# Performance work log

Hardware: AMD Instinct MI355X
Metric: run time of the kernel (lower is better)

Reference implementation:

```python
import jax, jax.numpy as jnp
import numpy as np

# Model dims (mamba-2.8b-ish layer, single 8192-token prefill)
H, I, N, R, K, L = 2048, 4096, 16, 128, 4, 8192


def setup_inputs() -> dict:
    key = jax.random.key(0)
    ks = jax.random.split(key, 7)
    return {
        "hidden_states": jax.random.normal(ks[0], (L, H), jnp.float32),
        "W_in": jax.random.normal(ks[1], (H, 2 * I), jnp.float32) * 0.02,   # in_proj (no bias)
        "conv_w": jax.random.normal(ks[2], (I, K), jnp.float32) * 0.2,      # depthwise conv weight
        "conv_b": jnp.zeros((I,), jnp.float32),                              # use_conv_bias=True
        "W_x": jax.random.normal(ks[3], (I, R + 2 * N), jnp.float32) * 0.02, # x_proj (no bias)
        "W_dt": jax.random.normal(ks[4], (R, I), jnp.float32) * 0.01,        # dt_proj weight
        "dt_bias": jax.random.normal(ks[5], (I,), jnp.float32) * 0.1,        # dt_proj bias (delta_bias)
        "A_log": jnp.log(jnp.broadcast_to(jnp.arange(1, N + 1, dtype=jnp.float32), (I, N))) + 0.0,
        "D": jnp.ones((I,), jnp.float32),
        "W_out": jax.random.normal(ks[6], (I, H), jnp.float32) * 0.02,       # out_proj (no bias)
    }


def silu(x):
    return x * jax.nn.sigmoid(x)


def causal_dw_conv(x, w, b):
    # x: [L, I]; depthwise causal conv along time (padding K-1, left only)
    xt = x.T[None]  # [1, I, L] (NCW)
    y = jax.lax.conv_general_dilated(xt, w[:, None, :], (1,), [(K - 1, 0)],
                                     feature_group_count=I)  # [1, I, L]
    return y[0].T + b


def mamba_forward(hidden_states, W_in, conv_w, conv_b, W_x, W_dt, dt_bias, A_log, D, W_out):
    proj = hidden_states @ W_in                     # [L, 2I]
    x, gate = proj[:, :I], proj[:, I:]
    x = silu(causal_dw_conv(x, conv_w, conv_b))     # causal_conv1d_fn with silu
    ssm = x @ W_x                                   # [L, R+2N]
    dt_lr, B, C = ssm[:, :R], ssm[:, R:R + N], ssm[:, R + N:]
    delta = jax.nn.softplus(dt_lr @ W_dt + dt_bias) # delta_softplus=True with delta_bias
    A = -jnp.exp(A_log)                             # [I, N]

    def step(h, t):
        d_t, B_t, C_t, u_t = t                      # [I], [N], [N], [I]
        h = h * jnp.exp(d_t[:, None] * A) + (d_t * u_t)[:, None] * B_t[None, :]
        return h, h @ C_t                           # y_t: [I]

    h0 = jnp.zeros((I, N), jnp.float32)
    _, y = jax.lax.scan(step, h0, (delta, B, C, x)) # y: [L, I]
    y = (y + x * D) * silu(gate)                    # skip D*u and z-gating (selective_scan_fn)
    return y @ W_out                                # out_proj -> [L, H]


def reference(hidden_states, W_in, conv_w, conv_b, W_x, W_dt, dt_bias, A_log, D, W_out):
    return mamba_forward(hidden_states, W_in, conv_w, conv_b, W_x, W_dt, dt_bias, A_log, D, W_out)
```

## Files before the change

### kernel.cpp

```cpp
#include <hip/hip_runtime.h>
#include <cmath>
#include <stdint.h>

#define H_DIM 2048
#define I_DIM 4096
#define N_DIM 16
#define R_DIM 128
#define K_CONV 4
#define L_DIM 8192
#define LC 2048
#define NCHUNK (L_DIM / LC)
#define SEG 32
#define TSEG (LC / SEG)
#define IN_DIM (I_DIM * N_DIM)

typedef _Float16 f16x8 __attribute__((ext_vector_type(8)));
typedef _Float16 f16x4v __attribute__((ext_vector_type(4)));
typedef float    f32x4 __attribute__((ext_vector_type(4)));

__device__ __forceinline__ void gl_lds(const _Float16* g, _Float16* lbase, int lane) {
#if __has_builtin(__builtin_amdgcn_global_load_lds)
    __builtin_amdgcn_global_load_lds(
        (const __attribute__((address_space(1))) void*)g,
        (__attribute__((address_space(3))) void*)lbase, 16, 0, 0);
#else
    *(f16x8*)&lbase[lane * 8] = *(const f16x8*)g;
#endif
}

template <int OUTF16>
__global__ __launch_bounds__(512, 1) void gemm_p256(
    const _Float16* __restrict__ Aph,
    const _Float16* __restrict__ Bph,
    void* __restrict__ Cv, int ldc, int Kd, int gm,
    int kchunk, size_t partStride)
{
    __shared__ __align__(16) _Float16 Sh[3][2][8192];

    const int tid = threadIdx.x;
    int bid = blockIdx.x;
    const int q = gridDim.x >> 3;
    bid = (bid & 7) * q + (bid >> 3);
    const int m0 = (bid % gm) * 256;
    const int n0 = (bid / gm) * 256;

    const int kbeg = blockIdx.y * kchunk;

    const int w = tid >> 6, l = tid & 63;
    const int wm = w & 3, wn = w >> 2;
    const int lr = l & 15, lg = l >> 4;

    const int KP = Kd >> 5;
    const int np0 = n0 >> 4, mp0 = m0 >> 4;
    const int st0 = w;

    f32x4 acc[4][8];
#pragma unroll
    for (int a = 0; a < 4; ++a)
#pragma unroll
        for (int b = 0; b < 8; ++b) acc[a][b] = (f32x4){0.f, 0.f, 0.f, 0.f};

    auto stage = [&](int k0, int p) {
        const int kp = k0 >> 5;
#pragma unroll
        for (int s = 0; s < 2; ++s) {
            const int st = st0 + s * 8;
            gl_lds(Aph + ((size_t)(mp0 + st) * KP + kp) * 512 + (size_t)l * 8,
                   &Sh[p][0][st * 512], l);
            gl_lds(Bph + ((size_t)(np0 + st) * KP + kp) * 512 + (size_t)l * 8,
                   &Sh[p][1][st * 512], l);
        }
    };
    auto domfma = [&](int b) {
        f16x8 fah[4];
#pragma unroll
        for (int t = 0; t < 4; ++t)
            fah[t] = *(const f16x8*)&Sh[b][0][(wm * 4 + t) * 512 + l * 8];
        __builtin_amdgcn_s_setprio(1);
#pragma unroll
        for (int nh = 0; nh < 2; ++nh) {
            f16x8 fbh[4];
#pragma unroll
            for (int t = 0; t < 4; ++t)
                fbh[t] = *(const f16x8*)&Sh[b][1][(wn * 8 + nh * 4 + t) * 512 + l * 8];
#pragma unroll
            for (int mt = 0; mt < 4; ++mt)
#pragma unroll
                for (int nt = 0; nt < 4; ++nt)
                    acc[mt][nh * 4 + nt] = __builtin_amdgcn_mfma_f32_16x16x32_f16(
                        fah[mt], fbh[nt], acc[mt][nh * 4 + nt], 0, 0, 0);
        }
        __builtin_amdgcn_s_setprio(0);
    };

    const int KT = kchunk >> 5;
    stage(kbeg, 0);
    stage(kbeg + 32, 1);
    for (int k = 0; k + 2 < KT; ++k) {
        stage(kbeg + (k + 2) * 32, (k + 2) % 3);
        asm volatile("s_waitcnt vmcnt(8)" ::: "memory");
        __builtin_amdgcn_s_barrier();
        __builtin_amdgcn_sched_barrier(0);
        domfma(k % 3);
        __builtin_amdgcn_s_barrier();
    }
    asm volatile("s_waitcnt vmcnt(4)" ::: "memory");
    __builtin_amdgcn_s_barrier();
    __builtin_amdgcn_sched_barrier(0);
    domfma((KT - 2) % 3);
    __builtin_amdgcn_s_barrier();
    asm volatile("s_waitcnt vmcnt(0)" ::: "memory");
    __builtin_amdgcn_s_barrier();
    __builtin_amdgcn_sched_barrier(0);
    domfma((KT - 1) % 3);

#pragma unroll
    for (int mt = 0; mt < 4; ++mt) {
        const int row = m0 + wm * 64 + mt * 16 + lg * 4;
#pragma unroll
        for (int nt = 0; nt < 8; ++nt) {
            const int col = n0 + wn * 128 + nt * 16 + lr;
#pragma unroll
            for (int j = 0; j < 4; ++j) {
                if (OUTF16) {
                    _Float16* C = (_Float16*)Cv + (size_t)blockIdx.y * partStride;
                    C[(size_t)(row + j) * ldc + col] = (_Float16)acc[mt][nt][j];
                } else {
                    float* C = (float*)Cv + (size_t)blockIdx.y * partStride;
                    C[(size_t)(row + j) * ldc + col] = acc[mt][nt][j];
                }
            }
        }
    }
}

__global__ __launch_bounds__(256) void reduce4_f16_kernel(
    const _Float16* __restrict__ P, float* __restrict__ out)
{
    const size_t idx = ((size_t)blockIdx.x * 256 + threadIdx.x) * 8;
    const size_t S = (size_t)LC * H_DIM;
    const f16x8 a = *(const f16x8*)(P + idx);
    const f16x8 b = *(const f16x8*)(P + S + idx);
    const f16x8 c = *(const f16x8*)(P + 2 * S + idx);
    const f16x8 d = *(const f16x8*)(P + 3 * S + idx);
    float r[8];
#pragma unroll
    for (int j = 0; j < 8; ++j)
        r[j] = ((float)a[j] + (float)b[j]) + ((float)c[j] + (float)d[j]);
    *(float4*)(out + idx)     = *(float4*)&r[0];
    *(float4*)(out + idx + 4) = *(float4*)&r[4];
}

template <int EPI, int AK, int ASPLIT, int BSPLIT, bool ATOMIC, int OUTF16>
__global__ __launch_bounds__(256, ASPLIT ? 2 : (BSPLIT ? 3 : 4)) void gemm_p(
    const void* __restrict__ Av, int lda,
    const _Float16* __restrict__ Aph,
    const _Float16* __restrict__ Bph, const _Float16* __restrict__ Bpl,
    void* __restrict__ Cv, int ldc,
    int Kd, int Ncap, int gm, int kchunk,
    const float* __restrict__ bias)
{
    constexpr int S_AH = 0;
    constexpr int S_AL = ASPLIT ? 1 : 0;
    constexpr int S_BH = ASPLIT ? 2 : 1;
    constexpr int S_BL = S_BH + 1;
    constexpr int NSLOT = S_BH + 1 + BSPLIT;
    __shared__ __align__(16) _Float16 Sh[2][NSLOT][4096];

    const int tid = threadIdx.x;
    int bid = blockIdx.x;
    const int q = gridDim.x >> 3;
    bid = (bid & 7) * q + (bid >> 3);
    const int m0 = (bid % gm) * 128;
    const int n0 = (bid / gm) * 128;

    const int kbeg = blockIdx.y * kchunk;
    const int kend = (kbeg + kchunk < Kd) ? (kbeg + kchunk) : Kd;

    const int w = tid >> 6, l = tid & 63;
    const int wm = w & 1, wn = w >> 1;
    const int lr = l & 15, lg = l >> 4;

    const int ar = tid >> 1, ah = tid & 1;
    const int aw0 = (ar >> 4) * 512 + (((ah * 2) * 16 + (ar & 15)) * 8);
    const int aw1 = aw0 + 128;

    const int KP = Kd >> 5;
    const int np0 = n0 >> 4;

    f32x4 acc[4][4];
#pragma unroll
    for (int a = 0; a < 4; ++a)
#pragma unroll
        for (int b = 0; b < 4; ++b) acc[a][b] = (f32x4){0.f, 0.f, 0.f, 0.f};

    float xf[16];
    f16x8 sah[2], sal[2];

    auto issueA = [&](int k0) {
        if (AK == 0) {
            const float* Ap = (const float*)Av + (size_t)(m0 + ar) * lda + k0 + ah * 16;
            *(float4*)&xf[0]  = *(const float4*)(Ap + 0);
            *(float4*)&xf[4]  = *(const float4*)(Ap + 4);
            *(float4*)&xf[8]  = *(const float4*)(Ap + 8);
            *(float4*)&xf[12] = *(const float4*)(Ap + 12);
        } else if (AK == 3) {
            const _Float16* Ap = (const _Float16*)Av + (size_t)(m0 + ar) * lda + k0 + ah * 16;
            sah[0] = *(const f16x8*)(Ap + 0);
            sah[1] = *(const f16x8*)(Ap + 8);
        }
    };
    auto cvtA = [&]() {
        if (AK == 0) {
#pragma unroll
            for (int c2 = 0; c2 < 2; ++c2)
#pragma unroll
                for (int j = 0; j < 8; ++j) {
                    const float xv = xf[c2 * 8 + j];
                    const _Float16 h = (_Float16)xv;
                    sah[c2][j] = h;
                    if (ASPLIT) sal[c2][j] = (_Float16)(xv - (float)h);
                }
        }
    };
    auto writeA = [&](int p) {
        *(f16x8*)&Sh[p][S_AH][aw0] = sah[0];
        *(f16x8*)&Sh[p][S_AH][aw1] = sah[1];
        if (ASPLIT) {
            *(f16x8*)&Sh[p][S_AL][aw0] = sal[0];
            *(f16x8*)&Sh[p][S_AL][aw1] = sal[1];
        }
    };
    auto stageGL = [&](int k0, int p) {
        const int kp = k0 >> 5;
#pragma unroll
        for (int qq = 0; qq < 2; ++qq) {
            const int st = 2 * w + qq;
            const size_t go = ((size_t)(np0 + st) * KP + kp) * 512 + (size_t)l * 8;
            gl_lds(Bph + go, &Sh[p][S_BH][st * 512], l);
            if (BSPLIT) gl_lds(Bpl + go, &Sh[p][S_BL][st * 512], l);
        }
    };
    auto domfma = [&](int b) {
        f16x8 fah[4], fal[4], fbh[4], fbl[4];
#pragma unroll
        for (int t = 0; t < 4; ++t) {
            fah[t] = *(const f16x8*)&Sh[b][S_AH][(wm * 4 + t) * 512 + l * 8];
            if (ASPLIT) fal[t] = *(const f16x8*)&Sh[b][S_AL][(wm * 4 + t) * 512 + l * 8];
            fbh[t] = *(const f16x8*)&Sh[b][S_BH][(wn * 4 + t) * 512 + l * 8];
            if (BSPLIT) fbl[t] = *(const f16x8*)&Sh[b][S_BL][(wn * 4 + t) * 512 + l * 8];
        }
        __builtin_amdgcn_s_setprio(1);
#pragma unroll
        for (int mt = 0; mt < 4; ++mt)
#pragma unroll
            for (int nt = 0; nt < 4; ++nt) {
                f32x4& a = acc[mt][nt];
                a = __builtin_amdgcn_mfma_f32_16x16x32_f16(fah[mt], fbh[nt], a, 0, 0, 0);
                if (BSPLIT)
                    a = __builtin_amdgcn_mfma_f32_16x16x32_f16(fah[mt], fbl[nt], a, 0, 0, 0);
                if (ASPLIT)
                    a = __builtin_amdgcn_mfma_f32_16x16x32_f16(fal[mt], fbh[nt], a, 0, 0, 0);
            }
        __builtin_amdgcn_s_setprio(0);
    };

    issueA(kbeg); cvtA(); writeA(0);
    stageGL(kbeg, 0);
    __syncthreads();
    int p = 0;
    for (int k0 = kbeg; k0 < kend; k0 += 32) {
        const bool more = (k0 + 32 < kend);
        if (more) {
            issueA(k0 + 32);
            stageGL(k0 + 32, p ^ 1);
        }
        domfma(p);
        if (more) { cvtA(); writeA(p ^ 1); }
        __syncthreads();
        p ^= 1;
    }

#pragma unroll
    for (int mt = 0; mt < 4; ++mt) {
        const int row = m0 + wm * 64 + mt * 16 + lg * 4;
#pragma unroll
        for (int nt = 0; nt < 4; ++nt) {
            const int col = n0 + wn * 64 + nt * 16 + lr;
            if (Ncap == 0 || col < Ncap) {
#pragma unroll
                for (int j = 0; j < 4; ++j) {
                    float v = acc[mt][nt][j];
                    if (EPI == 1) {
                        v += bias[col];
                        v = (v > 20.f) ? v : __logf(1.f + __expf(v));
                    }
                    const size_t off = (size_t)(row + j) * ldc + col;
                    if (ATOMIC)      atomicAdd(&((float*)Cv)[off], v);
                    else if (OUTF16) ((_Float16*)Cv)[off] = (_Float16)v;
                    else             ((float*)Cv)[off] = v;
                }
            }
        }
    }
}

__global__ __launch_bounds__(128) void pack_bp(
    const float* __restrict__ W, _Float16* __restrict__ Ph,
    _Float16* __restrict__ Pl, int Kd, int Nd)
{
    __shared__ float t[32][33];
    const int tid = threadIdx.x;
    const int n0 = blockIdx.x * 32, k0 = blockIdx.y * 32;
#pragma unroll
    for (int h = 0; h < 2; ++h) {
        const int qd = tid + h * 128;
        const int kk = qd >> 3, qq = qd & 7;
        *(float4*)&t[kk][qq * 4] = *(const float4*)(W + (size_t)(k0 + kk) * Nd + n0 + qq * 4);
    }
    __syncthreads();
    const int c = tid >> 5, nn = tid & 31;
    const int np = (n0 + nn) >> 4;
    const int r  = nn & 15;
    const int kp = k0 >> 5;
    const size_t base = ((size_t)np * (Kd >> 5) + kp) * 512 + (c * 16 + r) * 8;
    f16x8 vh, vl;
#pragma unroll
    for (int j = 0; j < 8; ++j) {
        const float v = t[c * 8 + j][nn];
        const _Float16 h = (_Float16)v;
        vh[j] = h;
        vl[j] = (_Float16)(v - (float)h);
    }
    *(f16x8*)&Ph[base] = vh;
    if (Pl) *(f16x8*)&Pl[base] = vl;
}

__global__ __launch_bounds__(256) void pack_ap(
    const float* __restrict__ A, int lda,
    _Float16* __restrict__ Ph, int Kd)
{
    const int tid = threadIdx.x;
    const int mp = blockIdx.x;
    const int r = tid >> 4, c8 = tid & 15;
    const int k0 = blockIdx.y * 128 + c8 * 8;
    const float* Ap = A + (size_t)(mp * 16 + r) * lda + k0;
    const float4 v0 = *(const float4*)Ap;
    const float4 v1 = *(const float4*)(Ap + 4);
    const float x[8] = {v0.x, v0.y, v0.z, v0.w, v1.x, v1.y, v1.z, v1.w};
    f16x8 vh;
#pragma unroll
    for (int j = 0; j < 8; ++j) vh[j] = (_Float16)x[j];
    const int kp = k0 >> 5;
    const int c  = (k0 >> 3) & 3;
    const size_t base = ((size_t)mp * (Kd >> 5) + kp) * 512 + (c * 16 + r) * 8;
    *(f16x8*)&Ph[base] = vh;
}

__global__ __launch_bounds__(256) void conv_silu_kernel(
    const _Float16* __restrict__ proj,
    const float* __restrict__ xtail_in,
    float* __restrict__ xtail_out,
    const float* __restrict__ w,
    const float* __restrict__ b,
    _Float16* __restrict__ xconv,
    float* __restrict__ ssm,
    int first)
{
    const int gid = blockIdx.x * 256 + threadIdx.x;
    if (gid < (LC * 160) / 4)
        *(float4*)(ssm + (size_t)gid * 4) = make_float4(0.f, 0.f, 0.f, 0.f);

    const int i4 = gid & (I_DIM / 4 - 1);
    const int t8 = gid >> 10;
    const int i = i4 * 4;
    const int tt0 = t8 * 8;

    const float4 w0 = *(const float4*)(w + (size_t)(i + 0) * 4);
    const float4 w1 = *(const float4*)(w + (size_t)(i + 1) * 4);
    const float4 w2 = *(const float4*)(w + (size_t)(i + 2) * 4);
    const float4 w3 = *(const float4*)(w + (size_t)(i + 3) * 4);
    const float4 bb = *(const float4*)(b + i);

    auto ldrow = [&](int row) -> float4 {
        const f16x4v v = *(const f16x4v*)(proj + (size_t)row * (2 * I_DIM) + i);
        return make_float4((float)v[0], (float)v[1], (float)v[2], (float)v[3]);
    };

    float4 r[11];
    if (tt0 >= 3) {
#pragma unroll
        for (int s = 0; s < 11; ++s) r[s] = ldrow(tt0 - 3 + s);
    } else {
#pragma unroll
        for (int s = 0; s < 3; ++s)
            r[s] = first ? make_float4(0.f, 0.f, 0.f, 0.f)
                         : *(const float4*)(xtail_in + (size_t)s * I_DIM + i);
#pragma unroll
        for (int s = 3; s < 11; ++s) r[s] = ldrow(tt0 - 3 + s);
    }

#pragma unroll
    for (int s = 0; s < 8; ++s) {
        float4 y = bb;
        y.x = fmaf(w0.x, r[s].x, y.x); y.x = fmaf(w0.y, r[s+1].x, y.x);
        y.x = fmaf(w0.z, r[s+2].x, y.x); y.x = fmaf(w0.w, r[s+3].x, y.x);
        y.y = fmaf(w1.x, r[s].y, y.y); y.y = fmaf(w1.y, r[s+1].y, y.y);
        y.y = fmaf(w1.z, r[s+2].y, y.y); y.y = fmaf(w1.w, r[s+3].y, y.y);
        y.z = fmaf(w2.x, r[s].z, y.z); y.z = fmaf(w2.y, r[s+1].z, y.z);
        y.z = fmaf(w2.z, r[s+2].z, y.z); y.z = fmaf(w2.w, r[s+3].z, y.z);
        y.w = fmaf(w3.x, r[s].w, y.w); y.w = fmaf(w3.y, r[s+1].w, y.w);
        y.w = fmaf(w3.z, r[s+2].w, y.w); y.w = fmaf(w3.w, r[s+3].w, y.w);
        y.x = y.x / (1.f + __expf(-y.x));
        y.y = y.y / (1.f + __expf(-y.y));
        y.z = y.z / (1.f + __expf(-y.z));
        y.w = y.w / (1.f + __expf(-y.w));
        f16x4v o;
        o[0] = (_Float16)y.x; o[1] = (_Float16)y.y;
        o[2] = (_Float16)y.z; o[3] = (_Float16)y.w;
        *(f16x4v*)(xconv + (size_t)(tt0 + s) * I_DIM + i) = o;
    }

    if (tt0 == LC - 8) {
#pragma unroll
        for (int qq = 0; qq < 3; ++qq)
            *(float4*)(xtail_out + (size_t)qq * I_DIM + i) = r[8 + qq];
    }
}

__global__ __launch_bounds__(256) void scan_part1(
    const _Float16* __restrict__ delta,
    const float* __restrict__ ssm,
    const _Float16* __restrict__ xc,
    const float* __restrict__ A_log,
    float* __restrict__ aprod,
    float* __restrict__ hend)
{
    __shared__ float Bs[TSEG][16];
    const int tid = threadIdx.x;
    const int i = blockIdx.x * 128 + (tid >> 1);
    const int half = tid & 1;
    const int seg = blockIdx.y;
    const int t0 = seg * TSEG;

    {
        const int tt = tid >> 2, c = (tid & 3) * 4;
        *(float4*)&Bs[tt][c] = *(const float4*)&ssm[(size_t)(t0 + tt) * 160 + 128 + c];
    }
    __syncthreads();

    float Ai[8], h[8], ap[8];
    {
        const float4 a0 = *(const float4*)&A_log[(size_t)i * 16 + half * 8];
        const float4 a1 = *(const float4*)&A_log[(size_t)i * 16 + half * 8 + 4];
        const float al[8] = {a0.x, a0.y, a0.z, a0.w, a1.x, a1.y, a1.z, a1.w};
#pragma unroll
        for (int n = 0; n < 8; ++n) { Ai[n] = -expf(al[n]); h[n] = 0.f; ap[n] = 1.f; }
    }

    float d0 = (float)delta[(size_t)t0 * (2 * I_DIM) + i];
    float u0 = (float)xc[(size_t)t0 * I_DIM + i];
    float d1 = (float)delta[(size_t)(t0 + 1) * (2 * I_DIM) + i];
    float u1 = (float)xc[(size_t)(t0 + 1) * I_DIM + i];
    for (int t = 0; t < TSEG; t += 2) {
        float d2 = 0.f, u2 = 0.f, d3 = 0.f, u3 = 0.f;
        if (t + 3 < TSEG) {
            d2 = (float)delta[(size_t)(t0 + t + 2) * (2 * I_DIM) + i];
            u2 = (float)xc[(size_t)(t0 + t + 2) * I_DIM + i];
            d3 = (float)delta[(size_t)(t0 + t + 3) * (2 * I_DIM) + i];
            u3 = (float)xc[(size_t)(t0 + t + 3) * I_DIM + i];
        }
        {
            const float du = d0 * u0;
#pragma unroll
            for (int n = 0; n < 8; ++n) {
                const float a = __expf(d0 * Ai[n]);
                h[n] = fmaf(h[n], a, du * Bs[t][half * 8 + n]);
                ap[n] *= a;
            }
        }
        {
            const float du = d1 * u1;
#pragma unroll
            for (int n = 0; n < 8; ++n) {
                const float a = __expf(d1 * Ai[n]);
                h[n] = fmaf(h[n], a, du * Bs[t + 1][half * 8 + n]);
                ap[n] *= a;
            }
        }
        d0 = d2; u0 = u2; d1 = d3; u1 = u3;
    }

    const size_t base = (size_t)seg * IN_DIM + (size_t)i * 16 + half * 8;
#pragma unroll
    for (int qq = 0; qq < 2; ++qq) {
        float4 va = {ap[qq * 4 + 0], ap[qq * 4 + 1], ap[qq * 4 + 2], ap[qq * 4 + 3]};
        float4 vh = {h[qq * 4 + 0], h[qq * 4 + 1], h[qq * 4 + 2], h[qq * 4 + 3]};
        *(float4*)&aprod[base + qq * 4] = va;
        *(float4*)&hend[base + qq * 4]  = vh;
    }
}

__global__ __launch_bounds__(256) void scan_part2(
    const float* __restrict__ aprod,
    float* __restrict__ hend,
    float* __restrict__ hstate,
    int first)
{
    const int gid = blockIdx.x * 256 + threadIdx.x;
    float h = first ? 0.f : hstate[gid];
    for (int s = 0; s < SEG; ++s) {
        const int idx = s * IN_DIM + gid;
        const float ap = aprod[idx];
        const float he = hend[idx];
        hend[idx] = h;
        h = fmaf(ap, h, he);
    }
    hstate[gid] = h;
}

__global__ __launch_bounds__(256) void scan_part3(
    const _Float16* __restrict__ delta,
    const _Float16* __restrict__ gate,
    const float* __restrict__ ssm,
    const _Float16* __restrict__ xc,
    _Float16* __restrict__ zPh,
    const float* __restrict__ A_log,
    const float* __restrict__ Dp,
    const float* __restrict__ hstart)
{
    __shared__ float BCs[TSEG][32];
    const int tid = threadIdx.x;
    const int i = blockIdx.x * 128 + (tid >> 1);
    const int half = tid & 1;
    const int seg = blockIdx.y;
    const int t0 = seg * TSEG;

    {
        const int tt = tid >> 2, c = (tid & 3) * 8;
        *(float4*)&BCs[tt][c]     = *(const float4*)&ssm[(size_t)(t0 + tt) * 160 + 128 + c];
        *(float4*)&BCs[tt][c + 4] = *(const float4*)&ssm[(size_t)(t0 + tt) * 160 + 132 + c];
    }
    __syncthreads();

    float Ai[8], h[8];
    {
        const float4 a0 = *(const float4*)&A_log[(size_t)i * 16 + half * 8];
        const float4 a1 = *(const float4*)&A_log[(size_t)i * 16 + half * 8 + 4];
        const float al[8] = {a0.x, a0.y, a0.z, a0.w, a1.x, a1.y, a1.z, a1.w};
#pragma unroll
        for (int n = 0; n < 8; ++n) Ai[n] = -expf(al[n]);
        const size_t base = (size_t)seg * IN_DIM + (size_t)i * 16 + half * 8;
        const float4 h0 = *(const float4*)&hstart[base];
        const float4 h1 = *(const float4*)&hstart[base + 4];
        h[0] = h0.x; h[1] = h0.y; h[2] = h0.z; h[3] = h0.w;
        h[4] = h1.x; h[5] = h1.y; h[6] = h1.z; h[7] = h1.w;
    }
    const float Di = Dp[i];

    const int kp = i >> 5, cc = (i >> 3) & 3, jj = i & 7;
    const size_t zb = (size_t)kp * 512 + (size_t)cc * 128 + jj;

    float d0 = (float)delta[(size_t)t0 * (2 * I_DIM) + i];
    float u0 = (float)xc[(size_t)t0 * I_DIM + i];
    float g0 = (float)gate[(size_t)t0 * (2 * I_DIM) + i];
    float d1 = (float)delta[(size_t)(t0 + 1) * (2 * I_DIM) + i];
    float u1 = (float)xc[(size_t)(t0 + 1) * I_DIM + i];
    float g1 = (float)gate[(size_t)(t0 + 1) * (2 * I_DIM) + i];
    for (int t = 0; t < TSEG; t += 2) {
        float d2 = 0.f, u2 = 0.f, g2 = 0.f, d3 = 0.f, u3 = 0.f, g3 = 0.f;
        if (t + 3 < TSEG) {
            d2 = (float)delta[(size_t)(t0 + t + 2) * (2 * I_DIM) + i];
            u2 = (float)xc[(size_t)(t0 + t + 2) * I_DIM + i];
            g2 = (float)gate[(size_t)(t0 + t + 2) * (2 * I_DIM) + i];
            d3 = (float)delta[(size_t)(t0 + t + 3) * (2 * I_DIM) + i];
            u3 = (float)xc[(size_t)(t0 + t + 3) * I_DIM + i];
            g3 = (float)gate[(size_t)(t0 + t + 3) * (2 * I_DIM) + i];
        }
#pragma unroll
        for (int ss = 0; ss < 2; ++ss) {
            const float d = ss ? d1 : d0;
            const float u = ss ? u1 : u0;
            const float g = ss ? g1 : g0;
            const int tt = t + ss;
            const float du = d * u;
            float y = 0.f;
#pragma unroll
            for (int n = 0; n < 8; ++n) {
                const float a = __expf(d * Ai[n]);
                h[n] = fmaf(h[n], a, du * BCs[tt][half * 8 + n]);
                y = fmaf(h[n], BCs[tt][16 + half * 8 + n], y);
            }
            y += __shfl_xor(y, 1);
            if (half == 0) {
                const float sg = g / (1.f + __expf(-g));
                const float zv = (y + u * Di) * sg;
                const int row = t0 + tt;
                zPh[((size_t)(row >> 4) * (I_DIM >> 5)) * 512 + zb + (size_t)(row & 15) * 8]
                    = (_Float16)zv;
            }
        }
        d0 = d2; u0 = u2; g0 = g2; d1 = d3; u1 = u3; g1 = g3;
    }
}

extern "C" void kernel_launch(void* const* d_in, const int* in_sizes, int n_in,
                              void* d_out, int out_size, void* d_ws, size_t ws_size,
                              hipStream_t stream)
{
    const float* hs      = (const float*)d_in[0];
    const float* W_in    = (const float*)d_in[1];
    const float* conv_w  = (const float*)d_in[2];
    const float* conv_b  = (const float*)d_in[3];
    const float* W_x     = (const float*)d_in[4];
    const float* W_dt    = (const float*)d_in[5];
    const float* dt_bias = (const float*)d_in[6];
    const float* A_log   = (const float*)d_in[7];
    const float* Dp      = (const float*)d_in[8];
    const float* W_out   = (const float*)d_in[9];
    float* out = (float*)d_out;

    char* p = (char*)d_ws;
    auto alloc = [&](size_t bytes) {
        char* r = p;
        p += (bytes + 255) & ~(size_t)255;
        return r;
    };
    _Float16* proj16 = (_Float16*)alloc((size_t)36 * 1024 * 1024);
    _Float16* xconv16 = (_Float16*)alloc((size_t)LC * I_DIM * 2);
    float* ssm    = (float*)alloc((size_t)LC * 160 * 4);
    float* xtail  = (float*)alloc((size_t)2 * 3 * I_DIM * 4);
    float* hstate = (float*)alloc((size_t)IN_DIM * 4);
    _Float16* WinPh  = (_Float16*)alloc((size_t)2 * I_DIM * H_DIM * 2);
    _Float16* WoutPh = (_Float16*)alloc((size_t)H_DIM * I_DIM * 2);
    _Float16* WdtPh  = (_Float16*)alloc((size_t)I_DIM * R_DIM * 2);
    _Float16* WdtPl  = (_Float16*)alloc((size_t)I_DIM * R_DIM * 2);
    _Float16* WxPh   = (_Float16*)alloc((size_t)256 * I_DIM * 2);
    _Float16* WxPl   = (_Float16*)alloc((size_t)256 * I_DIM * 2);
    _Float16* hsPh   = (_Float16*)alloc((size_t)L_DIM * H_DIM * 2);
    _Float16* zPh    = (_Float16*)alloc((size_t)LC * I_DIM * 2);

    const dim3 blk(256);
    const int NSSM = R_DIM + 2 * N_DIM;

    pack_bp<<<dim3(2 * I_DIM / 32, H_DIM / 32), dim3(128), 0, stream>>>(
        W_in, WinPh, nullptr, H_DIM, 2 * I_DIM);
    pack_bp<<<dim3(H_DIM / 32, I_DIM / 32), dim3(128), 0, stream>>>(
        W_out, WoutPh, nullptr, I_DIM, H_DIM);
    pack_bp<<<dim3(I_DIM / 32, R_DIM / 32), dim3(128), 0, stream>>>(
        W_dt, WdtPh, WdtPl, R_DIM, I_DIM);
    pack_bp<<<dim3(NSSM / 32, I_DIM / 32), dim3(128), 0, stream>>>(
        W_x, WxPh, WxPl, I_DIM, NSSM);
    pack_ap<<<dim3(L_DIM / 16, H_DIM / 128), blk, 0, stream>>>(
        hs, H_DIM, hsPh, H_DIM);

    for (int c = 0; c < NCHUNK; ++c) {
        const int t0 = c * LC;
        const int first = (c == 0) ? 1 : 0;
        float* out_c = out + (size_t)t0 * H_DIM;
        float* aprod = out_c;
        float* hend  = out_c + (size_t)SEG * IN_DIM;
        float* xtA = xtail + (size_t)(c & 1) * 3 * I_DIM;
        float* xtB = xtail + (size_t)((c & 1) ^ 1) * 3 * I_DIM;
        const _Float16* hsPh_c = hsPh + (size_t)(t0 >> 4) * (H_DIM >> 5) * 512;

        gemm_p256<1><<<dim3(256, 1), dim3(512), 0, stream>>>(
            hsPh_c, WinPh, proj16, 2 * I_DIM, H_DIM, LC / 256, H_DIM, 0);

        conv_silu_kernel<<<dim3(1024), blk, 0, stream>>>(
            proj16, xtA, xtB, conv_w, conv_b, xconv16, ssm, first);

        gemm_p<0, 3, 0, 1, true, 0><<<dim3(32, 8), blk, 0, stream>>>(
            xconv16, I_DIM, nullptr, WxPh, WxPl, ssm, NSSM,
            I_DIM, NSSM, LC / 128, I_DIM / 8, nullptr);

        gemm_p<1, 0, 1, 1, false, 1><<<dim3(512, 1), blk, 0, stream>>>(
            ssm, NSSM, nullptr, WdtPh, WdtPl, proj16, 2 * I_DIM,
            R_DIM, 0, LC / 128, R_DIM, dt_bias);

        scan_part1<<<dim3(I_DIM / 128, SEG), blk, 0, stream>>>(
            proj16, ssm, xconv16, A_log, aprod, hend);
        scan_part2<<<dim3(IN_DIM / 256), blk, 0, stream>>>(
            aprod, hend, hstate, first);
        scan_part3<<<dim3(I_DIM / 128, SEG), blk, 0, stream>>>(
            proj16, proj16 + I_DIM, ssm, xconv16, zPh, A_log, Dp, hend);

        gemm_p256<1><<<dim3(64, 4), dim3(512), 0, stream>>>(
            zPh, WoutPh, proj16, H_DIM, I_DIM, H_DIM / 256,
            I_DIM / 4, (size_t)LC * H_DIM);

        reduce4_f16_kernel<<<dim3(LC * H_DIM / 2048), blk, 0, stream>>>(
            proj16, out_c);
    }
}
```

Baseline: 1.047 ms.

## Load GEMM A fragments into registers and double the sequence chunk length

```diff
diff --git a/kernel.cpp b/kernel.cpp
--- a/kernel.cpp
+++ b/kernel.cpp
@@ -8,9 +8,9 @@
 #define R_DIM 128
 #define K_CONV 4
 #define L_DIM 8192
-#define LC 2048
+#define LC 4096
 #define NCHUNK (L_DIM / LC)
-#define SEG 32
+#define SEG 64
 #define TSEG (LC / SEG)
 #define IN_DIM (I_DIM * N_DIM)
 
@@ -29,13 +29,13 @@
 }
 
 template <int OUTF16>
-__global__ __launch_bounds__(512, 1) void gemm_p256(
+__global__ __launch_bounds__(512, 1) void gemm_r256(
     const _Float16* __restrict__ Aph,
     const _Float16* __restrict__ Bph,
     void* __restrict__ Cv, int ldc, int Kd, int gm,
     int kchunk, size_t partStride)
 {
-    __shared__ __align__(16) _Float16 Sh[3][2][8192];
+    __shared__ __align__(16) _Float16 Bs[3][8192];
 
     const int tid = threadIdx.x;
     int bid = blockIdx.x;
@@ -43,7 +43,6 @@
     bid = (bid & 7) * q + (bid >> 3);
     const int m0 = (bid % gm) * 256;
     const int n0 = (bid / gm) * 256;
-
     const int kbeg = blockIdx.y * kchunk;
 
     const int w = tid >> 6, l = tid & 63;
@@ -52,7 +51,6 @@
 
     const int KP = Kd >> 5;
     const int np0 = n0 >> 4, mp0 = m0 >> 4;
-    const int st0 = w;
 
     f32x4 acc[4][8];
 #pragma unroll
@@ -60,59 +58,74 @@
 #pragma unroll
         for (int b = 0; b < 8; ++b) acc[a][b] = (f32x4){0.f, 0.f, 0.f, 0.f};
 
-    auto stage = [&](int k0, int p) {
+    const _Float16* Abase = Aph + ((size_t)(mp0 + wm * 4) * KP) * 512 + (size_t)l * 8;
+    const size_t Astride = (size_t)KP * 512;
+
+    f16x8 faA[4], faB[4];
+
+    auto loadA = [&](int k0, f16x8* fa) {
+        const size_t ko = (size_t)(k0 >> 5) * 512;
+#pragma unroll
+        for (int t = 0; t < 4; ++t)
+            fa[t] = *(const f16x8*)(Abase + (size_t)t * Astride + ko);
+    };
+    auto stageB = [&](int k0, int p) {
         const int kp = k0 >> 5;
 #pragma unroll
         for (int s = 0; s < 2; ++s) {
-            const int st = st0 + s * 8;
-            gl_lds(Aph + ((size_t)(mp0 + st) * KP + kp) * 512 + (size_t)l * 8,
-                   &Sh[p][0][st * 512], l);
+            const int st = w + s * 8;
             gl_lds(Bph + ((size_t)(np0 + st) * KP + kp) * 512 + (size_t)l * 8,
-                   &Sh[p][1][st * 512], l);
-        }
-    };
-    auto domfma = [&](int b) {
-        f16x8 fah[4];
-#pragma unroll
-        for (int t = 0; t < 4; ++t)
-            fah[t] = *(const f16x8*)&Sh[b][0][(wm * 4 + t) * 512 + l * 8];
+                   &Bs[p][st * 512], l);
+        }
+    };
+    auto domfma = [&](int p, f16x8* fa) {
+        f16x8 fb[8];
+#pragma unroll
+        for (int nt = 0; nt < 8; ++nt)
+            fb[nt] = *(const f16x8*)&Bs[p][(wn * 8 + nt) * 512 + l * 8];
         __builtin_amdgcn_s_setprio(1);
 #pragma unroll
-        for (int nh = 0; nh < 2; ++nh) {
-            f16x8 fbh[4];
-#pragma unroll
-            for (int t = 0; t < 4; ++t)
-                fbh[t] = *(const f16x8*)&Sh[b][1][(wn * 8 + nh * 4 + t) * 512 + l * 8];
-#pragma unroll
-            for (int mt = 0; mt < 4; ++mt)
-#pragma unroll
-                for (int nt = 0; nt < 4; ++nt)
-                    acc[mt][nh * 4 + nt] = __builtin_amdgcn_mfma_f32_16x16x32_f16(
-                        fah[mt], fbh[nt], acc[mt][nh * 4 + nt], 0, 0, 0);
-        }
+        for (int mt = 0; mt < 4; ++mt)
+#pragma unroll
+            for (int nt = 0; nt < 8; ++nt)
+                acc[mt][nt] = __builtin_amdgcn_mfma_f32_16x16x32_f16(
+                    fa[mt], fb[nt], acc[mt][nt], 0, 0, 0);
         __builtin_amdgcn_s_setprio(0);
     };
 
     const int KT = kchunk >> 5;
-    stage(kbeg, 0);
-    stage(kbeg + 32, 1);
-    for (int k = 0; k + 2 < KT; ++k) {
-        stage(kbeg + (k + 2) * 32, (k + 2) % 3);
+    stageB(kbeg, 0);
+    stageB(kbeg + 32, 1);
+    loadA(kbeg, faA);
+
+    int k = 0;
+    for (; k + 3 < KT; k += 2) {
+        stageB(kbeg + (k + 2) * 32, (k + 2) % 3);
+        loadA(kbeg + (k + 1) * 32, faB);
         asm volatile("s_waitcnt vmcnt(8)" ::: "memory");
         __builtin_amdgcn_s_barrier();
         __builtin_amdgcn_sched_barrier(0);
-        domfma(k % 3);
+        domfma(k % 3, faA);
         __builtin_amdgcn_s_barrier();
-    }
+
+        stageB(kbeg + (k + 3) * 32, (k + 3) % 3);
+        loadA(kbeg + (k + 2) * 32, faA);
+        asm volatile("s_waitcnt vmcnt(8)" ::: "memory");
+        __builtin_amdgcn_s_barrier();
+        __builtin_amdgcn_sched_barrier(0);
+        domfma((k + 1) % 3, faB);
+        __builtin_amdgcn_s_barrier();
+    }
+    loadA(kbeg + (KT - 1) * 32, faB);
     asm volatile("s_waitcnt vmcnt(4)" ::: "memory");
     __builtin_amdgcn_s_barrier();
     __builtin_amdgcn_sched_barrier(0);
-    domfma((KT - 2) % 3);
+    domfma((KT - 2) % 3, faA);
     __builtin_amdgcn_s_barrier();
     asm volatile("s_waitcnt vmcnt(0)" ::: "memory");
     __builtin_amdgcn_s_barrier();
     __builtin_amdgcn_sched_barrier(0);
-    domfma((KT - 1) % 3);
+    domfma((KT - 1) % 3, faB);
 
 #pragma unroll
     for (int mt = 0; mt < 4; ++mt) {
@@ -510,7 +523,7 @@
     const int gid = blockIdx.x * 256 + threadIdx.x;
     float h = first ? 0.f : hstate[gid];
     for (int s = 0; s < SEG; ++s) {
-        const int idx = s * IN_DIM + gid;
+        const size_t idx = (size_t)s * IN_DIM + gid;
         const float ap = aprod[idx];
         const float he = hend[idx];
         hend[idx] = h;
@@ -626,7 +639,7 @@
         p += (bytes + 255) & ~(size_t)255;
         return r;
     };
-    _Float16* proj16 = (_Float16*)alloc((size_t)36 * 1024 * 1024);
+    _Float16* proj16 = (_Float16*)alloc((size_t)68 * 1024 * 1024);
     _Float16* xconv16 = (_Float16*)alloc((size_t)LC * I_DIM * 2);
     float* ssm    = (float*)alloc((size_t)LC * 160 * 4);
     float* xtail  = (float*)alloc((size_t)2 * 3 * I_DIM * 4);
@@ -664,17 +677,17 @@
         float* xtB = xtail + (size_t)((c & 1) ^ 1) * 3 * I_DIM;
         const _Float16* hsPh_c = hsPh + (size_t)(t0 >> 4) * (H_DIM >> 5) * 512;
 
-        gemm_p256<1><<<dim3(256, 1), dim3(512), 0, stream>>>(
+        gemm_r256<1><<<dim3(512, 1), dim3(512), 0, stream>>>(
             hsPh_c, WinPh, proj16, 2 * I_DIM, H_DIM, LC / 256, H_DIM, 0);
 
-        conv_silu_kernel<<<dim3(1024), blk, 0, stream>>>(
+        conv_silu_kernel<<<dim3((LC / 8) * (I_DIM / 4) / 256), blk, 0, stream>>>(
             proj16, xtA, xtB, conv_w, conv_b, xconv16, ssm, first);
 
-        gemm_p<0, 3, 0, 1, true, 0><<<dim3(32, 8), blk, 0, stream>>>(
+        gemm_p<0, 3, 0, 1, true, 0><<<dim3(2 * (LC / 128), 8), blk, 0, stream>>>(
             xconv16, I_DIM, nullptr, WxPh, WxPl, ssm, NSSM,
             I_DIM, NSSM, LC / 128, I_DIM / 8, nullptr);
 
-        gemm_p<1, 0, 1, 1, false, 1><<<dim3(512, 1), blk, 0, stream>>>(
+        gemm_p<1, 0, 1, 1, false, 1><<<dim3(32 * (LC / 128), 1), blk, 0, stream>>>(
             ssm, NSSM, nullptr, WdtPh, WdtPl, proj16, 2 * I_DIM,
             R_DIM, 0, LC / 128, R_DIM, dt_bias);
 
@@ -685,8 +698,8 @@
         scan_part3<<<dim3(I_DIM / 128, SEG), blk, 0, stream>>>(
             proj16, proj16 + I_DIM, ssm, xconv16, zPh, A_log, Dp, hend);
 
-        gemm_p256<1><<<dim3(64, 4), dim3(512), 0, stream>>>(
-            zPh, WoutPh, proj16, H_DIM, I_DIM, H_DIM / 256,
+        gemm_r256<1><<<dim3((LC / 256) * (H_DIM / 256), 4), dim3(512), 0, stream>>>(
+            zPh, WoutPh, proj16, H_DIM, I_DIM, LC / 256,
             I_DIM / 4, (size_t)LC * H_DIM);
 
         reduce4_f16_kernel<<<dim3(LC * H_DIM / 2048), blk, 0, stream>>>(
```

Measured after the change: 1.022 ms. 1.02x faster.
